# Kernel optimization log

Hardware: AMD Instinct MI355X
Metric: run time of the kernel (lower is better)

Reference implementation:

```python
import jax, jax.numpy as jnp
import numpy as np

N_UNITS = 512
N_HEADS = 8
CHUNK = N_UNITS // N_HEADS
SCALE = 1.0 / (CHUNK ** 0.5)


def setup_inputs() -> dict:
    key = jax.random.key(0)
    k1, k2, k3, k4, k5, k6 = jax.random.split(key, 6)
    B, Nx, Ny = 8, 1024, 1024
    x = jax.random.normal(k1, (B, N_UNITS, Nx), dtype=jnp.float32)
    y = jax.random.normal(k2, (B, N_UNITS, Ny), dtype=jnp.float32)
    xy_mask = jax.random.randint(k3, (B, Nx, Ny), 0, 2) > 0
    # conv1x1 weight [out, in] (ConvolutionSentence, bias=False)
    W = jax.random.normal(k4, (N_UNITS, N_UNITS), dtype=jnp.float32) * (1.0 / np.sqrt(N_UNITS))
    fc_w = jax.random.normal(k5, (1, N_HEADS), dtype=jnp.float32) * (1.0 / np.sqrt(N_HEADS))
    fc_b = jax.random.normal(k6, (1,), dtype=jnp.float32) * 0.01
    return {"x": x, "y": y, "xy_mask": xy_mask, "W": W, "fc_w": fc_w, "fc_b": fc_b}


def reference(x, y, xy_mask, W, fc_w, fc_b):
    B, U, Nx = x.shape
    Ny = y.shape[2]
    H, C = N_HEADS, CHUNK
    # 1x1 conv over channel dim == linear on channels
    _x = jnp.einsum('oi,bin->bon', W, x)  # [B, U, Nx]
    _y = jnp.einsum('oi,bim->bom', W, y)  # [B, U, Ny]
    # split channels into heads (contiguous chunks, matching torch.split)
    xh = _x.reshape(B, H, C, Nx)
    yh = _y.reshape(B, H, C, Ny)
    # per-head scores: relu, then scale, then mask (order matches torch code)
    s = jnp.einsum('bhcn,bhcm->bhnm', xh, yh)  # [B, H, Nx, Ny]
    s = jnp.maximum(s, 0.0) * SCALE
    s = jnp.where(xy_mask[:, None, :, :], s, 0.0)
    similarity = s.sum(axis=(2, 3))  # [B, H]
    n_el = xy_mask.sum(axis=(1, 2))
    n_el = jnp.where(n_el == 0, 1, n_el).astype(similarity.dtype)
    expectation = similarity / n_el[:, None]
    return expectation @ fc_w.T + fc_b  # [B, 1]
```

## Files before the change

kernel.cpp:

```cpp
#include <hip/hip_runtime.h>
#include <stdint.h>

#define UU 512
#define NHEAD 8
#define NB 8
#define NXX 1024
#define NYY 1024
#define SCALE_F 0.125f

typedef __bf16 bf16x8 __attribute__((ext_vector_type(8)));
typedef float f32x4 __attribute__((ext_vector_type(4)));
typedef unsigned short us4 __attribute__((ext_vector_type(4)));

__device__ __forceinline__ unsigned short f2bf(float f) {
  union { float f; uint32_t u; } v; v.f = f;
  return (unsigned short)((v.u + 0x7FFFu + ((v.u >> 16) & 1u)) >> 16);
}

__global__ void prep_kernel(const float* __restrict__ W, unsigned short* __restrict__ Wb,
                            const unsigned char* __restrict__ m, int* __restrict__ det) {
  int blk = blockIdx.x, t = threadIdx.x;
  if (blk < 1024) {
    int i = blk * 256 + t;
    Wb[i] = f2bf(W[i]);
  } else {
    int idx = ((blk - 1024) * 256 + t) * 16;
    uint4 v = *(const uint4*)(m + idx);
    unsigned int c1 = (v.x & 0xff00u) | (v.y & 0xff00u) | (v.z & 0xff00u) | (v.w & 0xff00u);
    if (c1) atomicOr(&det[0], 1);
  }
}

__global__ __launch_bounds__(256, 4) void conv_fused(
    const float* __restrict__ x, const float* __restrict__ y,
    const unsigned short* __restrict__ Wb, unsigned short* __restrict__ cv) {
  __shared__ unsigned short xs[32 * 512];
  int fl = blockIdx.x;
  int bz = fl & 15, nt = (fl >> 4) & 31, ut = fl >> 9;
  int b = bz & 7;
  const float* src = (bz >> 3) ? y : x;
  int n0 = nt * 32;
  int t = threadIdx.x, w = t >> 6, l = t & 63;
  int lane_m = l & 15, lane_g = l >> 4;

  {
    int cq = (t & 7) * 4;
    int i2b = (t >> 3) * 2;
    const float* gb = src + (size_t)b * UU * NXX + n0 + cq;
#pragma unroll
    for (int it = 0; it < 8; it++) {
      int i2 = i2b + it * 64;
      float4 va = *(const float4*)(gb + (size_t)i2 * NXX);
      float4 vb = *(const float4*)(gb + (size_t)(i2 + 1) * NXX);
#pragma unroll
      for (int j = 0; j < 4; j++) {
        int n = cq + j;
        unsigned int pk = (unsigned int)f2bf(((const float*)&va)[j])
                        | ((unsigned int)f2bf(((const float*)&vb)[j]) << 16);
        int e = n * 512 + (i2 ^ ((n & 7) << 3));
        *(unsigned int*)&xs[e] = pk;
      }
    }
  }
  __syncthreads();

  int u0 = ut * 256 + w * 64;
  const unsigned short* wb0 = Wb + (size_t)u0 * UU;
  f32x4 acc[2][4] = {};
  bf16x8 aA[4], aB[4], bA[2], bB[2];

#define LOADW(Adst, Bdst, KB) do {                                            \
    int k_ = (KB) * 32 + lane_g * 8;                                          \
    _Pragma("unroll") for (int tu = 0; tu < 4; tu++)                          \
      Adst[tu] = *(const bf16x8*)(wb0 + (size_t)(tu * 16 + lane_m) * UU + k_);\
    _Pragma("unroll") for (int tn = 0; tn < 2; tn++) {                        \
      int nl_ = tn * 16 + lane_m;                                             \
      Bdst[tn] = *(const bf16x8*)&xs[nl_ * 512 + (k_ ^ ((nl_ & 7) << 3))];    \
    }                                                                         \
  } while (0)
#define DOMFMA(Ab, Bb) do {                                                   \
    _Pragma("unroll") for (int tn = 0; tn < 2; tn++)                          \
    _Pragma("unroll") for (int tu = 0; tu < 4; tu++)                          \
      acc[tn][tu] = __builtin_amdgcn_mfma_f32_16x16x32_bf16(Ab[tu], Bb[tn], acc[tn][tu], 0, 0, 0); \
  } while (0)

  LOADW(aA, bA, 0);
#pragma unroll
  for (int kp = 0; kp < 8; kp++) {
    LOADW(aB, bB, 2 * kp + 1);
    DOMFMA(aA, bA);
    if (kp < 7) LOADW(aA, bA, 2 * kp + 2);
    DOMFMA(aB, bB);
  }
#undef LOADW
#undef DOMFMA

  unsigned short* ob = cv + (size_t)bz * NXX * UU;
#pragma unroll
  for (int tn = 0; tn < 2; tn++)
#pragma unroll
    for (int tu = 0; tu < 4; tu++) {
      int n = n0 + tn * 16 + lane_m;
      int u = u0 + tu * 16 + 4 * lane_g;
      us4 pk;
      pk.x = f2bf(acc[tn][tu][0]); pk.y = f2bf(acc[tn][tu][1]);
      pk.z = f2bf(acc[tn][tu][2]); pk.w = f2bf(acc[tn][tu][3]);
      *(us4*)(ob + (size_t)n * UU + u) = pk;
    }
}

__global__ __launch_bounds__(256, 2) void score_kernel(
    const unsigned short* __restrict__ cv, const void* __restrict__ maskp,
    const int* __restrict__ det, float* __restrict__ part) {
  __shared__ unsigned short ys[64 * 512];
  __shared__ unsigned short mf16[64][72];
  __shared__ float red[4][8];
  int fl = blockIdx.x;
  int b = fl & 7, rr = fl >> 3;
  int nt = rr & 15, mt = rr >> 4;
  int t = threadIdx.x, w = t >> 6, l = t & 63;
  int lane_m = l & 15, lane_g = l >> 4;
  int n0 = nt * 64, m0 = mt * 64;
  int nw0 = (w & 1) * 32, hq = (w >> 1) * 4;

  const unsigned short* xb = cv + ((size_t)b * NXX + n0 + nw0) * UU;
  bf16x8 afr[4][2][2];
#pragma unroll
  for (int hh = 0; hh < 4; hh++) {
    int co = (hq + hh) * 64;
#pragma unroll
    for (int tn = 0; tn < 2; tn++)
#pragma unroll
      for (int kb = 0; kb < 2; kb++)
        afr[hh][tn][kb] = *(const bf16x8*)(xb + (size_t)(tn * 16 + lane_m) * UU + co + kb * 32 + lane_g * 8);
  }

  const unsigned short* yb = cv + ((size_t)(NB + b) * NYY + m0) * UU;
  {
    int seg = t & 63;
#pragma unroll
    for (int p = 0; p < 16; p++) {
      int r2 = p * 4 + (t >> 6);
      uint4 v = *(const uint4*)(yb + (size_t)r2 * UU + seg * 8);
      int sp = seg ^ (r2 & 7);
      *(uint4*)&ys[r2 * 512 + sp * 8] = v;
    }
  }

  int is_u8 = det[0] != 0;
  unsigned int cl = 0;
  {
    int row = t >> 2, cq = (t & 3) * 16;
    size_t eb = ((size_t)b * NXX + n0 + row) * NYY + m0 + cq;
    if (is_u8) {
      uint4 v = *(const uint4*)((const unsigned char*)maskp + eb);
#pragma unroll
      for (int j = 0; j < 16; j++) {
        unsigned int word = ((const unsigned int*)&v)[j >> 2];
        int bit = ((word >> ((j & 3) * 8)) & 0xffu) != 0;
        mf16[row][cq + j] = bit ? 0x3F80u : 0u;
        cl += (unsigned)bit;
      }
    } else {
      const unsigned int* mp = (const unsigned int*)maskp + eb;
#pragma unroll
      for (int q = 0; q < 4; q++) {
        uint4 v = *(const uint4*)(mp + q * 4);
        unsigned int wds[4] = {v.x, v.y, v.z, v.w};
#pragma unroll
        for (int j = 0; j < 4; j++) {
          int bit = wds[j] != 0;
          mf16[row][cq + q * 4 + j] = bit ? 0x3F80u : 0u;
          cl += (unsigned)bit;
        }
      }
    }
  }
  for (int s = 1; s < 64; s <<= 1) cl += __shfl_xor(cl, s);
  if (l == 0) red[w][4] = (float)cl;
  __syncthreads();

  float mreg[2][4][4];
#pragma unroll
  for (int tn = 0; tn < 2; tn++)
#pragma unroll
    for (int tm = 0; tm < 4; tm++)
#pragma unroll
      for (int r = 0; r < 4; r++) {
        unsigned int u = (unsigned int)mf16[nw0 + tn * 16 + 4 * lane_g + r][tm * 16 + lane_m] << 16;
        union { unsigned int u; float f; } cvt; cvt.u = u;
        mreg[tn][tm][r] = cvt.f;
      }

  float hsv[4] = {0.f, 0.f, 0.f, 0.f};
#pragma unroll
  for (int hh = 0; hh < 4; hh++) {
    int segbase = (hq + hh) * 8;
    bf16x8 bfr[4][2];
#pragma unroll
    for (int tm = 0; tm < 4; tm++) {
      int row = tm * 16 + lane_m;
#pragma unroll
      for (int kb = 0; kb < 2; kb++) {
        int sp = (segbase + kb * 4 + lane_g) ^ (row & 7);
        bfr[tm][kb] = *(const bf16x8*)&ys[row * 512 + sp * 8];
      }
    }
#pragma unroll
    for (int tn = 0; tn < 2; tn++)
#pragma unroll
      for (int tm = 0; tm < 4; tm++) {
        f32x4 acc = {};
        acc = __builtin_amdgcn_mfma_f32_16x16x32_bf16(afr[hh][tn][0], bfr[tm][0], acc, 0, 0, 0);
        acc = __builtin_amdgcn_mfma_f32_16x16x32_bf16(afr[hh][tn][1], bfr[tm][1], acc, 0, 0, 0);
#pragma unroll
        for (int r = 0; r < 4; r++) {
          float v = acc[r];
          v = v > 0.f ? v : 0.f;
          hsv[hh] = fmaf(v, mreg[tn][tm][r], hsv[hh]);
        }
      }
  }
#pragma unroll
  for (int hh = 0; hh < 4; hh++) {
    float hs = hsv[hh];
    for (int s = 1; s < 64; s <<= 1) hs += __shfl_xor(hs, s);
    if (l == 0) red[w][hh] = hs;
  }
  __syncthreads();
  float* pb = part + (size_t)fl * 16;
  if (t < 8) {
    int q = t >> 2, hh = t & 3;
    pb[t] = red[q * 2][hh] + red[q * 2 + 1][hh];
  } else if (t == 8) {
    pb[8] = red[0][4] + red[1][4] + red[2][4] + red[3][4];
  }
}

__global__ __launch_bounds__(256) void finalize(
    const float* __restrict__ part, const float* __restrict__ fcw,
    const float* __restrict__ fcb, float* __restrict__ out) {
  __shared__ float red[4][9];
  int b = blockIdx.x;
  int t = threadIdx.x, w = t >> 6, l = t & 63;
  const float* pb = part + (size_t)(t * 8 + b) * 16;
  float v[9];
#pragma unroll
  for (int j = 0; j < 9; j++) v[j] = pb[j];
#pragma unroll
  for (int j = 0; j < 9; j++) {
    float s = v[j];
    for (int ss = 1; ss < 64; ss <<= 1) s += __shfl_xor(s, ss);
    v[j] = s;
  }
  if (l == 0)
#pragma unroll
    for (int j = 0; j < 9; j++) red[w][j] = v[j];
  __syncthreads();
  if (t == 0) {
    float s = 0.f, cn = 0.f;
#pragma unroll
    for (int h = 0; h < NHEAD; h++)
      s += (red[0][h] + red[1][h] + red[2][h] + red[3][h]) * fcw[h];
    cn = red[0][8] + red[1][8] + red[2][8] + red[3][8];
    if (cn < 0.5f) cn = 1.f;
    out[b] = s * (SCALE_F / cn) + fcb[0];
  }
}

extern "C" void kernel_launch(void* const* d_in, const int* in_sizes, int n_in,
                              void* d_out, int out_size, void* d_ws, size_t ws_size,
                              hipStream_t stream) {
  const float* x = (const float*)d_in[0];
  const float* y = (const float*)d_in[1];
  const void* mask = d_in[2];
  const float* W = (const float*)d_in[3];
  const float* fcw = (const float*)d_in[4];
  const float* fcb = (const float*)d_in[5];
  float* out = (float*)d_out;
  char* ws = (char*)d_ws;

  unsigned short* cv = (unsigned short*)ws;
  unsigned short* Wb = (unsigned short*)(ws + (16u << 20));
  float* part = (float*)(ws + (16u << 20) + (1u << 19));
  char* st = ws + (16u << 20) + (1u << 19) + (1u << 17);
  int* det = (int*)st;

  hipMemsetAsync(st, 0, 64, stream);
  prep_kernel<<<1040, 256, 0, stream>>>(W, Wb, (const unsigned char*)mask, det);
  conv_fused<<<1024, 256, 0, stream>>>(x, y, Wb, cv);
  score_kernel<<<2048, 256, 0, stream>>>(cv, mask, det, part);
  finalize<<<NB, 256, 0, stream>>>(part, fcw, fcb, out);
}
```

Measured before the change: 166.9 us.

## Pre-pack W into MFMA fragment layout and double conv N-tile to 64

The prep kernel now converts W to bf16 in a fragment-ordered layout, so each lane's A-operand load in the conv kernel is one contiguous 16-byte read and a wavefront's loads are fully coalesced. The conv kernel's N tile grows from 32 to 64 columns, giving a 4x4 MFMA accumulator block per wave. This halves the number of blocks that reload W and doubles reuse of each loaded W fragment. The cost is double the LDS (64 KB) and more registers, with launch bounds lowered to 2 blocks per SM, which reduces occupancy.

```diff
diff --git a/kernel.cpp b/kernel.cpp
--- a/kernel.cpp
+++ b/kernel.cpp
@@ -17,46 +17,57 @@
   return (unsigned short)((v.u + 0x7FFFu + ((v.u >> 16) & 1u)) >> 16);
 }
 
-__global__ void prep_kernel(const float* __restrict__ W, unsigned short* __restrict__ Wb,
+__global__ void prep_kernel(const float* __restrict__ W, unsigned short* __restrict__ Wp,
                             const unsigned char* __restrict__ m, int* __restrict__ det) {
   int blk = blockIdx.x, t = threadIdx.x;
-  if (blk < 1024) {
-    int i = blk * 256 + t;
-    Wb[i] = f2bf(W[i]);
+  if (blk < 128) {
+    int s = blk * 256 + t;
+    int ub = s >> 10, kb = (s >> 6) & 15, l = s & 63;
+    int u = ub * 16 + (l & 15), k = kb * 32 + (l >> 4) * 8;
+    const float* src = W + (size_t)u * UU + k;
+    float4 a = *(const float4*)src;
+    float4 bq = *(const float4*)(src + 4);
+    uint4 o;
+    o.x = (unsigned)f2bf(a.x) | ((unsigned)f2bf(a.y) << 16);
+    o.y = (unsigned)f2bf(a.z) | ((unsigned)f2bf(a.w) << 16);
+    o.z = (unsigned)f2bf(bq.x) | ((unsigned)f2bf(bq.y) << 16);
+    o.w = (unsigned)f2bf(bq.z) | ((unsigned)f2bf(bq.w) << 16);
+    *(uint4*)(Wp + (size_t)s * 8) = o;
   } else {
-    int idx = ((blk - 1024) * 256 + t) * 16;
+    int idx = ((blk - 128) * 256 + t) * 16;
     uint4 v = *(const uint4*)(m + idx);
     unsigned int c1 = (v.x & 0xff00u) | (v.y & 0xff00u) | (v.z & 0xff00u) | (v.w & 0xff00u);
     if (c1) atomicOr(&det[0], 1);
   }
 }
 
-__global__ __launch_bounds__(256, 4) void conv_fused(
+__global__ __launch_bounds__(256, 2) void conv_fused(
     const float* __restrict__ x, const float* __restrict__ y,
-    const unsigned short* __restrict__ Wb, unsigned short* __restrict__ cv) {
-  __shared__ unsigned short xs[32 * 512];
+    const unsigned short* __restrict__ Wp, unsigned short* __restrict__ cv) {
+  __shared__ unsigned short xs[64 * 512];
   int fl = blockIdx.x;
-  int bz = fl & 15, nt = (fl >> 4) & 31, ut = fl >> 9;
+  int bz = fl & 15, nt = (fl >> 4) & 15, ut = fl >> 8;
   int b = bz & 7;
   const float* src = (bz >> 3) ? y : x;
-  int n0 = nt * 32;
+  int n0 = nt * 64;
   int t = threadIdx.x, w = t >> 6, l = t & 63;
   int lane_m = l & 15, lane_g = l >> 4;
 
   {
-    int cq = (t & 7) * 4;
-    int i2b = (t >> 3) * 2;
+    int cq = (t & 15) * 4;
+    int i2b = (t >> 4) * 2;
     const float* gb = src + (size_t)b * UU * NXX + n0 + cq;
 #pragma unroll
-    for (int it = 0; it < 8; it++) {
-      int i2 = i2b + it * 64;
+    for (int it = 0; it < 16; it++) {
+      int i2 = i2b + it * 32;
       float4 va = *(const float4*)(gb + (size_t)i2 * NXX);
       float4 vb = *(const float4*)(gb + (size_t)(i2 + 1) * NXX);
+      float fa[4] = {va.x, va.y, va.z, va.w};
+      float fb[4] = {vb.x, vb.y, vb.z, vb.w};
 #pragma unroll
       for (int j = 0; j < 4; j++) {
         int n = cq + j;
-        unsigned int pk = (unsigned int)f2bf(((const float*)&va)[j])
-                        | ((unsigned int)f2bf(((const float*)&vb)[j]) << 16);
+        unsigned int pk = (unsigned)f2bf(fa[j]) | ((unsigned)f2bf(fb[j]) << 16);
         int e = n * 512 + (i2 ^ ((n & 7) << 3));
         *(unsigned int*)&xs[e] = pk;
       }
@@ -65,21 +76,22 @@
   __syncthreads();
 
   int u0 = ut * 256 + w * 64;
-  const unsigned short* wb0 = Wb + (size_t)u0 * UU;
-  f32x4 acc[2][4] = {};
-  bf16x8 aA[4], aB[4], bA[2], bB[2];
+  int ub0 = u0 >> 4;
+  const unsigned short* wb0 = Wp + (size_t)l * 8;
+  f32x4 acc[4][4] = {};
+  bf16x8 aA[4], aB[4], bA[4], bB[4];
 
 #define LOADW(Adst, Bdst, KB) do {                                            \
-    int k_ = (KB) * 32 + lane_g * 8;                                          \
     _Pragma("unroll") for (int tu = 0; tu < 4; tu++)                          \
-      Adst[tu] = *(const bf16x8*)(wb0 + (size_t)(tu * 16 + lane_m) * UU + k_);\
-    _Pragma("unroll") for (int tn = 0; tn < 2; tn++) {                        \
+      Adst[tu] = *(const bf16x8*)(wb0 + ((size_t)(ub0 + tu) * 16 + (KB)) * 512); \
+    _Pragma("unroll") for (int tn = 0; tn < 4; tn++) {                        \
       int nl_ = tn * 16 + lane_m;                                             \
-      Bdst[tn] = *(const bf16x8*)&xs[nl_ * 512 + (k_ ^ ((nl_ & 7) << 3))];    \
+      int ka_ = (KB) * 32 + lane_g * 8;                                       \
+      Bdst[tn] = *(const bf16x8*)&xs[nl_ * 512 + (ka_ ^ ((nl_ & 7) << 3))];   \
     }                                                                         \
   } while (0)
 #define DOMFMA(Ab, Bb) do {                                                   \
-    _Pragma("unroll") for (int tn = 0; tn < 2; tn++)                          \
+    _Pragma("unroll") for (int tn = 0; tn < 4; tn++)                          \
     _Pragma("unroll") for (int tu = 0; tu < 4; tu++)                          \
       acc[tn][tu] = __builtin_amdgcn_mfma_f32_16x16x32_bf16(Ab[tu], Bb[tn], acc[tn][tu], 0, 0, 0); \
   } while (0)
@@ -97,7 +109,7 @@
 
   unsigned short* ob = cv + (size_t)bz * NXX * UU;
 #pragma unroll
-  for (int tn = 0; tn < 2; tn++)
+  for (int tn = 0; tn < 4; tn++)
 #pragma unroll
     for (int tu = 0; tu < 4; tu++) {
       int n = n0 + tn * 16 + lane_m;
@@ -281,14 +293,14 @@
   char* ws = (char*)d_ws;
 
   unsigned short* cv = (unsigned short*)ws;
-  unsigned short* Wb = (unsigned short*)(ws + (16u << 20));
+  unsigned short* Wp = (unsigned short*)(ws + (16u << 20));
   float* part = (float*)(ws + (16u << 20) + (1u << 19));
   char* st = ws + (16u << 20) + (1u << 19) + (1u << 17);
   int* det = (int*)st;
 
   hipMemsetAsync(st, 0, 64, stream);
-  prep_kernel<<<1040, 256, 0, stream>>>(W, Wb, (const unsigned char*)mask, det);
-  conv_fused<<<1024, 256, 0, stream>>>(x, y, Wb, cv);
+  prep_kernel<<<144, 256, 0, stream>>>(W, Wp, (const unsigned char*)mask, det);
+  conv_fused<<<512, 256, 0, stream>>>(x, y, Wp, cv);
   score_kernel<<<2048, 256, 0, stream>>>(cv, mask, det, part);
   finalize<<<NB, 256, 0, stream>>>(part, fcw, fcb, out);
 }
```

New measurement: 144.3 us. -13.6%, faster.
